# Optimization experiments

Measured on AMD Instinct MI355X. Metric: run time of the kernel, lower is better.

The kernel has to match this reference:

```python
import jax, jax.numpy as jnp
import numpy as np

P, M, N, D, H, DFF = 20000, 20000, 16, 128, 8, 512
DPH = D // H
EPS = 1e-6
LN_EPS = 1e-5


def vn_linear(x, w):
    # x: (..., C_in, 3), w: (C_in, C_out) -> (..., C_out, 3)
    return jnp.einsum('...ci,co->...oi', x, w)


def vn_layernorm(x, gamma, beta):
    # x: (P, D, 3); layernorm over channel dim on vector norms, rescale directions
    n = jnp.linalg.norm(x, axis=-1)                      # (P, D)
    mu = jnp.mean(n, axis=-1, keepdims=True)
    var = jnp.var(n, axis=-1, keepdims=True)
    n_hat = (n - mu) / jnp.sqrt(var + LN_EPS) * gamma + beta
    return x * (n_hat / (n + EPS))[..., None]


def vn_relu(q, k):
    # VN nonlinearity: q, k: (..., C, 3); project q off negative half-space of k
    dot = jnp.sum(q * k, axis=-1, keepdims=True)         # (..., C, 1)
    ksq = jnp.sum(k * k, axis=-1, keepdims=True)
    return jnp.where(dot >= 0, q, q - (dot / (ksq + EPS)) * k)


def setup_inputs():
    key = jax.random.key(0)
    ks = jax.random.split(key, 24)
    s = lambda i, shp, scale: (jax.random.normal(ks[i], shp, jnp.float32) * scale)
    inp = {
        'tgt': s(0, (P, D * 3), 1.0),
        'memory': s(1, (M, D * 3), 1.0),
        'sh': s(2, (P, N + 1, 3), 1.0),
        'dist_atten': s(3, (P, N, H), 1.0),
        'Wq': s(4, (D, D), D ** -0.5),
        'Wk': s(5, (D, D), D ** -0.5),
        'Wv': s(6, (D, D), D ** -0.5),
        'Wo': s(7, (D, D), D ** -0.5),
        'g_w1': s(8, (D, H), D ** -0.5),
        'g_b1': jnp.zeros((H,), jnp.float32),
        'g_w2': s(9, (H, H), H ** -0.5),
        'g_b2': jnp.zeros((H,), jnp.float32),
        'ln1_g': jnp.ones((D,), jnp.float32),
        'ln1_b': jnp.zeros((D,), jnp.float32),
        'ln2_g': jnp.ones((D,), jnp.float32),
        'ln2_b': jnp.zeros((D,), jnp.float32),
        'ff_w1': s(10, (D, DFF), D ** -0.5),
        'ff_d1': s(11, (D, DFF), D ** -0.5),
        'ff_w2': s(12, (DFF, D), DFF ** -0.5),
        'index_pair': jax.random.randint(ks[13], (P, N), 0, M),
        'cnt1': jax.random.randint(ks[14], (P,), 0, N),
        'cnt2': jax.random.randint(ks[15], (P,), 0, N),
    }
    return inp


def reference(tgt, memory, sh, dist_atten, Wq, Wk, Wv, Wo,
              g_w1, g_b1, g_w2, g_b2, ln1_g, ln1_b, ln2_g, ln2_b,
              ff_w1, ff_d1, ff_w2, index_pair, cnt1, cnt2):
    x = tgt.reshape(P, D, 3)
    mem = memory.reshape(M, D, 3)
    q = vn_linear(x, Wq)                                  # (P, D, 3)
    k_all = vn_linear(mem, Wk)                            # (M, D, 3)
    v_all = vn_linear(mem, Wv)
    # irregular neighbor gather (ca_attention_mapper_v3)
    k = k_all[index_pair]                                 # (P, N, D, 3)
    v = v_all[index_pair]                                 # (P, N, D, 3)
    sh_n = sh[:, 1:].reshape(P, N, 1, 3)                  # drop l=0 term
    # multi-head dot attention on 3D vector features
    dot_atten = jnp.einsum('phdi,pnhdi->pnh',
                           q.reshape(P, H, DPH, 3),
                           k.reshape(P, N, H, DPH, 3))
    # spherical-harmonic position bias
    pos = jnp.sum((k - q[:, None]) * sh_n, axis=-1)       # (P, N, D)
    pos = jax.nn.relu(pos @ g_w1 + g_b1) @ g_w2 + g_b2    # (P, N, H)
    atten = (dot_atten + pos + dist_atten) / (DPH ** 0.5)
    atten = jax.nn.softmax(atten, axis=1)                 # softmax over neighbors
    tgt2 = jnp.einsum('pnh,pnhci->phci', atten,
                      v.reshape(P, N, H, DPH, 3)).reshape(P, D, 3)
    tgt2 = vn_linear(tgt2, Wo)
    y = vn_layernorm(x + tgt2, ln1_g, ln1_b)
    h1 = vn_relu(vn_linear(y, ff_w1), vn_linear(y, ff_d1))
    ff_out = vn_linear(h1, ff_w2)
    y = vn_layernorm(y + ff_out, ln2_g, ln2_b)
    return y.reshape(P, D * 3)
```

## Files before the change

### kernel.cpp

```cpp
#include <hip/hip_runtime.h>

#define PP 20000

typedef short short8 __attribute__((ext_vector_type(8)));
typedef float floatx4 __attribute__((ext_vector_type(4)));

__device__ __forceinline__ unsigned int bf16_rne_bits(float x){
    unsigned int xb = __float_as_uint(x);
    return (xb + 0x7FFFu + ((xb >> 16) & 1u)) & 0xFFFF0000u;
}
__device__ __forceinline__ void split2(float x, short &h, short &l){
    unsigned int hb = bf16_rne_bits(x);
    h = (short)(hb >> 16);
    float r = x - __uint_as_float(hb);
    l = (short)(bf16_rne_bits(r) >> 16);
}

__device__ __align__(16) short g_ff1[32*8192];
__device__ __align__(16) short g_ff2[16*8192];
__device__ __align__(16) short g_qkvo[4][4*8192];

__global__ __launch_bounds__(256) void prep_weights(
    const float* __restrict__ Wq, const float* __restrict__ Wk,
    const float* __restrict__ Wv, const float* __restrict__ Wo,
    const float* __restrict__ W1, const float* __restrict__ Wd,
    const float* __restrict__ W2)
{
    const int tid = blockIdx.x*256 + threadIdx.x;
    for (int e = tid; e < 65536; e += 16384){
        int j = e & 7, kg = (e>>3) & 15, n = (e>>7) & 15, ch = e >> 11;
        int k = kg*8 + j, col = ch*16 + n;
        int pos = n*128 + ((kg ^ (n&7)) << 3) + j;
        short h, l;
        split2(W1[(size_t)k*512 + col], h, l);
        g_ff1[ch*8192 + pos]        = h;
        g_ff1[ch*8192 + 2048 + pos] = l;
        split2(Wd[(size_t)k*512 + col], h, l);
        g_ff1[ch*8192 + 4096 + pos] = h;
        g_ff1[ch*8192 + 6144 + pos] = l;
    }
    for (int e = tid; e < 65536; e += 16384){
        int w = e & 31, n2 = (e>>5) & 127, pair = e >> 12;
        int lslot = (w>>3) ^ ((n2>>1)&3);
        int k = pair*32 + lslot*8 + (w&7);
        short h, l; split2(W2[(size_t)k*128 + n2], h, l);
        g_ff2[pair*8192 + n2*32 + w]        = h;
        g_ff2[pair*8192 + 4096 + n2*32 + w] = l;
    }
    for (int e = tid; e < 65536; e += 16384){
        int w = e & 127, col = (e>>7) & 31, ch = (e>>12) & 3, wg = e >> 14;
        int lslot = (w>>3) ^ (col&7);
        int k = lslot*8 + (w&7);
        const float* Wsrc = (wg==0)?Wq:(wg==1)?Wk:(wg==2)?Wv:Wo;
        short h, l; split2(Wsrc[(size_t)k*128 + ch*32 + col], h, l);
        g_qkvo[wg][ch*8192 + col*128 + w]        = h;
        g_qkvo[wg][ch*8192 + 4096 + col*128 + w] = l;
    }
}

__global__ __launch_bounds__(256) void vn_gemm_mfma(const float* __restrict__ in,
    int widx, float* __restrict__ out)
{
    __shared__ __align__(16) char pool[32768];
    short* Ysh = (short*)pool;
    short* Ysl = (short*)(pool + 16384);
    short* Bh  = (short*)pool;
    short* Bl  = (short*)(pool + 8192);

    const int tid  = threadIdx.x;
    const int wv   = tid >> 6;
    const int lane = tid & 63;
    const int mrow = lane & 15;
    const int kgrp = lane >> 4;
    const int p0   = blockIdx.x * 16;

    for (int f = tid; f < 2048; f += 256){
        int row = (f >> 7)*4 + 3, k = f & 127;
        Ysh[row*128 + k] = 0; Ysl[row*128 + k] = 0;
    }
    #pragma unroll
    for (int t = 0; t < 6; ++t){
        int f = tid + t*256;
        float4 w4 = *(const float4*)(in + (size_t)p0*384 + f*4);
        int e = f*4, pl = e/384, rem = e - pl*384;
        float vv4[4] = {w4.x, w4.y, w4.z, w4.w};
        #pragma unroll
        for (int j=0;j<4;++j){
            int c = (rem+j)/3, i = (rem+j) - c*3;
            int row = pl*4 + i;
            int idx = row*128 + (((c>>3) ^ (row&7)) << 3) + (c&7);
            short h, l; split2(vv4[j], h, l);
            Ysh[idx] = h; Ysl[idx] = l;
        }
    }
    __syncthreads();
    short8 ahf[4], alf[4];
    {
        const int arow = wv*16 + mrow;
        #pragma unroll
        for (int ks=0;ks<4;++ks){
            int slot = ks*4 + kgrp;
            int aoff = arow*128 + ((slot ^ (arow&7)) << 3);
            ahf[ks] = *(const short8*)(Ysh + aoff);
            alf[ks] = *(const short8*)(Ysl + aoff);
        }
    }

    const short* gW = g_qkvo[widx];
    for (int ch = 0; ch < 4; ++ch){
        __syncthreads();
        #pragma unroll
        for (int t=0;t<4;++t)
            ((short8*)pool)[tid + t*256] =
                ((const short8*)(gW + ch*8192))[tid + t*256];
        __syncthreads();

        #pragma unroll
        for (int ntl=0; ntl<2; ++ntl){
            floatx4 acc = {0.f,0.f,0.f,0.f};
            const int lcol = ntl*16 + mrow;
            #pragma unroll
            for (int ks=0;ks<4;++ks){
                int slot = ks*4 + kgrp;
                int boff = lcol*128 + ((slot ^ (mrow&7)) << 3);
                short8 bh = *(const short8*)(Bh + boff);
                short8 bl = *(const short8*)(Bl + boff);
                acc = __builtin_amdgcn_mfma_f32_16x16x32_bf16(ahf[ks], bh, acc, 0,0,0);
                acc = __builtin_amdgcn_mfma_f32_16x16x32_bf16(ahf[ks], bl, acc, 0,0,0);
                acc = __builtin_amdgcn_mfma_f32_16x16x32_bf16(alf[ks], bh, acc, 0,0,0);
            }
            const int p = p0 + wv*4 + kgrp;
            const int o = ch*32 + ntl*16 + mrow;
            size_t base = (size_t)p*384 + (size_t)o*3;
            out[base    ] = acc[0];
            out[base + 1] = acc[1];
            out[base + 2] = acc[2];
        }
    }
}

__global__ __launch_bounds__(128) void attn_score(
    const float* qf, const float* __restrict__ kf,
    const float* __restrict__ sh, const float* __restrict__ dist, const int* __restrict__ idxp,
    const float* __restrict__ gw1, const float* __restrict__ gb1,
    const float* __restrict__ gw2, const float* __restrict__ gb2,
    float* att)
{
    const int p = blockIdx.x, c = threadIdx.x;
    __shared__ __align__(16) float dot_s[16*132];
    __shared__ __align__(16) float pos_s[16*132];
    __shared__ float sh_s[48];
    __shared__ int   nidx[16];
    __shared__ __align__(16) float w1t[8*132];
    __shared__ float w2_s[64], b1_s[8], b2_s[8];
    __shared__ float u2_s[16*8], logit_s[16*8];

    if (c < 16) nidx[c] = idxp[p*16 + c];
    if (c < 48) sh_s[c] = sh[(size_t)p*51 + 3 + c];
    #pragma unroll
    for (int f = c; f < 1024; f += 128){
        int th2 = f >> 7, cc2 = f & 127;
        w1t[th2*132 + cc2] = gw1[cc2*8 + th2];
    }
    if (c < 64) w2_s[c] = gw2[c];
    if (c < 8){ b1_s[c]=gb1[c]; b2_s[c]=gb2[c]; }
    size_t qa = (size_t)p*384 + c*3;
    float qx = qf[qa], qy = qf[qa+1], qz = qf[qa+2];
    __syncthreads();

    for (int n=0;n<16;++n){
        size_t kbase = (size_t)nidx[n]*384 + c*3;
        float kx = kf[kbase], ky = kf[kbase+1], kz = kf[kbase+2];
        dot_s[n*132 + c] = kx*qx + ky*qy + kz*qz;
        pos_s[n*132 + c] = (kx-qx)*sh_s[n*3] + (ky-qy)*sh_s[n*3+1] + (kz-qz)*sh_s[n*3+2];
    }
    __syncthreads();

    const int tn = c >> 3, th = c & 7;
    const float* drow = dot_s + tn*132 + th*16;
    float4 d0 = *(const float4*)(drow);
    float4 d1 = *(const float4*)(drow + 4);
    float4 d2 = *(const float4*)(drow + 8);
    float4 d3 = *(const float4*)(drow + 12);
    float dsum = (d0.x+d0.y+d0.z+d0.w) + (d1.x+d1.y+d1.z+d1.w)
               + (d2.x+d2.y+d2.z+d2.w) + (d3.x+d3.y+d3.z+d3.w);

    float uj = b1_s[th];
    const float* prow = pos_s + tn*132;
    const float* wrow = w1t  + th*132;
    #pragma unroll 8
    for (int cc=0; cc<128; cc+=4){
        float4 pv = *(const float4*)(prow + cc);
        float4 wv = *(const float4*)(wrow + cc);
        uj = fmaf(pv.x, wv.x, uj);
        uj = fmaf(pv.y, wv.y, uj);
        uj = fmaf(pv.z, wv.z, uj);
        uj = fmaf(pv.w, wv.w, uj);
    }
    u2_s[tn*8+th] = fmaxf(uj, 0.f);
    __syncthreads();

    float l = b2_s[th];
    #pragma unroll
    for (int j=0;j<8;++j) l += u2_s[tn*8+j]*w2_s[j*8+th];
    l += dsum + dist[(size_t)p*128 + tn*8 + th];
    logit_s[tn*8+th] = l * 0.25f;
    __syncthreads();

    if (c < 8){
        float mx = -3.0e38f;
        #pragma unroll
        for (int n=0;n<16;++n) mx = fmaxf(mx, logit_s[n*8+c]);
        float e[16], ssum = 0.f;
        #pragma unroll
        for (int n=0;n<16;++n){ e[n] = __expf(logit_s[n*8+c]-mx); ssum += e[n]; }
        float inv = 1.f/ssum;
        #pragma unroll
        for (int n=0;n<16;++n) att[(size_t)p*384 + n*8 + c] = e[n]*inv;
    }
}

__global__ __launch_bounds__(128) void attn_apply(const float* __restrict__ vv,
                                                  const int* __restrict__ idxp,
                                                  float* io)
{
    const int p = blockIdx.x, c = threadIdx.x;
    __shared__ float att_s[128];
    __shared__ int   nidx[16];
    if (c < 16) nidx[c] = idxp[p*16 + c];
    att_s[c] = io[(size_t)p*384 + c];
    __syncthreads();

    const int h = c >> 4;
    float ax=0.f, ay=0.f, az=0.f;
    #pragma unroll
    for (int n=0;n<16;++n){
        float wgt = att_s[n*8+h];
        size_t vb = (size_t)nidx[n]*384 + c*3;
        ax += wgt*vv[vb]; ay += wgt*vv[vb+1]; az += wgt*vv[vb+2];
    }
    size_t ob = (size_t)p*384 + c*3;
    io[ob] = ax; io[ob+1] = ay; io[ob+2] = az;
}

__global__ __launch_bounds__(256,2) void vn_ff_mfma(const float* __restrict__ in,
    const float* __restrict__ l2g, const float* __restrict__ l2b,
    float* __restrict__ out)
{
    __shared__ __align__(16) char pool[40960];
    short* Ws1h = (short*)(pool);
    short* Ws1l = (short*)(pool + 4096);
    short* Wsdh = (short*)(pool + 8192);
    short* Wsdl = (short*)(pool + 12288);
    short* Ws2h = (short*)(pool + 16384);
    short* Ws2l = (short*)(pool + 24576);
    short* Hsh  = (short*)(pool + 32768);
    short* Hsl  = (short*)(pool + 36864);
    short* Ysh  = (short*)(pool);
    short* Ysl  = (short*)(pool + 16384);

    const int tid  = threadIdx.x;
    const int wv   = tid >> 6;
    const int lane = tid & 63;
    const int mrow = lane & 15;
    const int kgrp = lane >> 4;
    const int p0   = blockIdx.x * 16;

    for (int f = tid; f < 2048; f += 256){
        int row = (f >> 7)*4 + 3, k = f & 127;
        Ysh[row*128 + k] = 0; Ysl[row*128 + k] = 0;
    }
    #pragma unroll
    for (int t = 0; t < 6; ++t){
        int f = tid + t*256;
        float4 w4 = *(const float4*)(in + (size_t)p0*384 + f*4);
        int e = f*4, pl = e/384, rem = e - pl*384;
        float vv4[4] = {w4.x, w4.y, w4.z, w4.w};
        #pragma unroll
        for (int j=0;j<4;++j){
            int c = (rem+j)/3, i = (rem+j) - c*3;
            int row = pl*4 + i;
            int idx = row*128 + (((c>>3) ^ (row&7)) << 3) + (c&7);
            short h, l; split2(vv4[j], h, l);
            Ysh[idx] = h; Ysl[idx] = l;
        }
    }
    __syncthreads();
    short8 ahf[4], alf[4];
    {
        const int arow = wv*16 + mrow;
        #pragma unroll
        for (int ks=0;ks<4;++ks){
            int slot = ks*4 + kgrp;
            int aoff = arow*128 + ((slot ^ (arow&7)) << 3);
            ahf[ks] = *(const short8*)(Ysh + aoff);
            alf[ks] = *(const short8*)(Ysl + aoff);
        }
    }

    floatx4 acc2[8];
    #pragma unroll
    for (int nt=0;nt<8;++nt) acc2[nt] = (floatx4){0.f,0.f,0.f,0.f};

    for (int ch = 0; ch < 32; ++ch){
        __syncthreads();
        #pragma unroll
        for (int t=0;t<4;++t)
            ((short8*)pool)[tid + t*256] =
                ((const short8*)(g_ff1 + ch*8192))[tid + t*256];
        if ((ch & 1) == 0){
            #pragma unroll
            for (int t=0;t<4;++t)
                ((short8*)(pool + 16384))[tid + t*256] =
                    ((const short8*)(g_ff2 + (ch>>1)*8192))[tid + t*256];
        }
        __syncthreads();

        floatx4 aU = {0.f,0.f,0.f,0.f}, aD = {0.f,0.f,0.f,0.f};
        #pragma unroll
        for (int ks=0;ks<4;++ks){
            int slot = ks*4 + kgrp;
            int boff = mrow*128 + ((slot ^ (mrow&7)) << 3);
            short8 b1h = *(const short8*)(Ws1h + boff);
            short8 b1l = *(const short8*)(Ws1l + boff);
            short8 bdh = *(const short8*)(Wsdh + boff);
            short8 bdl = *(const short8*)(Wsdl + boff);
            aU = __builtin_amdgcn_mfma_f32_16x16x32_bf16(ahf[ks], b1h, aU, 0,0,0);
            aU = __builtin_amdgcn_mfma_f32_16x16x32_bf16(ahf[ks], b1l, aU, 0,0,0);
            aU = __builtin_amdgcn_mfma_f32_16x16x32_bf16(alf[ks], b1h, aU, 0,0,0);
            aD = __builtin_amdgcn_mfma_f32_16x16x32_bf16(ahf[ks], bdh, aD, 0,0,0);
            aD = __builtin_amdgcn_mfma_f32_16x16x32_bf16(ahf[ks], bdl, aD, 0,0,0);
            aD = __builtin_amdgcn_mfma_f32_16x16x32_bf16(alf[ks], bdh, aD, 0,0,0);
        }

        {
            float ux=aU[0], uy=aU[1], uz=aU[2];
            float dx=aD[0], dy=aD[1], dz=aD[2];
            float dot = ux*dx + uy*dy + uz*dz;
            float ksq = dx*dx + dy*dy + dz*dz;
            if (dot < 0.f){
                float fc = dot/(ksq + 1e-6f);
                ux -= fc*dx; uy -= fc*dy; uz -= fc*dz;
            }
            int col  = (ch & 1)*16 + mrow;
            int slot = col >> 3, cl = col & 7;
            float hv[4] = {ux, uy, uz, 0.f};
            #pragma unroll
            for (int r=0;r<4;++r){
                int row = wv*16 + kgrp*4 + r;
                int idx = row*32 + ((slot ^ ((row>>1)&3)) << 3) + cl;
                short h, l; split2(hv[r], h, l);
                Hsh[idx] = h; Hsl[idx] = l;
            }
        }

        if (ch & 1){
            const int arow2 = wv*16 + mrow;
            int aoff = arow2*32 + ((kgrp ^ ((arow2>>1)&3)) << 3);
            short8 ah = *(const short8*)(Hsh + aoff);
            short8 al = *(const short8*)(Hsl + aoff);
            #pragma unroll
            for (int nt=0;nt<8;++nt){
                int bcol = nt*16 + mrow;
                int boff = bcol*32 + ((kgrp ^ ((bcol>>1)&3)) << 3);
                short8 bh = *(const short8*)(Ws2h + boff);
                short8 bl = *(const short8*)(Ws2l + boff);
                acc2[nt] = __builtin_amdgcn_mfma_f32_16x16x32_bf16(ah, bh, acc2[nt], 0,0,0);
                acc2[nt] = __builtin_amdgcn_mfma_f32_16x16x32_bf16(ah, bl, acc2[nt], 0,0,0);
                acc2[nt] = __builtin_amdgcn_mfma_f32_16x16x32_bf16(al, bh, acc2[nt], 0,0,0);
            }
        }
    }

    const int p = p0 + wv*4 + kgrp;
    float nrm[8];
    float s1 = 0.f, s2 = 0.f;
    #pragma unroll
    for (int nt=0;nt<8;++nt){
        int o = nt*16 + mrow;
        size_t base = (size_t)p*384 + (size_t)o*3;
        float rx = in[base]   + acc2[nt][0];
        float ry = in[base+1] + acc2[nt][1];
        float rz = in[base+2] + acc2[nt][2];
        float n = sqrtf(rx*rx + ry*ry + rz*rz);
        nrm[nt] = n;
        s1 += n; s2 += n*n;
    }
    #pragma unroll
    for (int m=1; m<16; m<<=1){
        s1 += __shfl_xor(s1, m);
        s2 += __shfl_xor(s2, m);
    }
    float mu  = s1*(1.f/128.f);
    float var = s2*(1.f/128.f) - mu*mu;
    float inv = rsqrtf(var + 1e-5f);
    #pragma unroll
    for (int nt=0;nt<8;++nt){
        int o = nt*16 + mrow;
        size_t base = (size_t)p*384 + (size_t)o*3;
        float rx = in[base]   + acc2[nt][0];
        float ry = in[base+1] + acc2[nt][1];
        float rz = in[base+2] + acc2[nt][2];
        float nh = (nrm[nt] - mu)*inv*l2g[o] + l2b[o];
        float sc = nh/(nrm[nt] + 1e-6f);
        out[base] = rx*sc; out[base+1] = ry*sc; out[base+2] = rz*sc;
    }
}

__global__ __launch_bounds__(256) void vn_ln(const float* __restrict__ a, const float* b2,
                                             const float* __restrict__ gamma, const float* __restrict__ beta,
                                             float* out)
{
    const int tid = threadIdx.x;
    const int pl = tid >> 7, c = tid & 127;
    const int p = blockIdx.x*2 + pl;
    size_t base = (size_t)p*384 + c*3;
    float rx = a[base]   + b2[base];
    float ry = a[base+1] + b2[base+1];
    float rz = a[base+2] + b2[base+2];
    float nc = sqrtf(rx*rx + ry*ry + rz*rz);
    float s1 = nc, s2 = nc*nc;
    for (int off=32; off; off>>=1){ s1 += __shfl_down(s1, off); s2 += __shfl_down(s2, off); }
    __shared__ float pr[4][2];
    if ((tid & 63) == 0){ pr[tid>>6][0] = s1; pr[tid>>6][1] = s2; }
    __syncthreads();
    float S1 = pr[pl*2][0] + pr[pl*2+1][0];
    float S2 = pr[pl*2][1] + pr[pl*2+1][1];
    float mu  = S1*(1.f/128.f);
    float var = S2*(1.f/128.f) - mu*mu;
    float nh = (nc - mu)*rsqrtf(var + 1e-5f)*gamma[c] + beta[c];
    float sc = nh/(nc + 1e-6f);
    out[base] = rx*sc; out[base+1] = ry*sc; out[base+2] = rz*sc;
}

extern "C" void kernel_launch(void* const* d_in, const int* in_sizes, int n_in,
                              void* d_out, int out_size, void* d_ws, size_t ws_size,
                              hipStream_t stream)
{
    const float* tgt  = (const float*)d_in[0];
    const float* mem  = (const float*)d_in[1];
    const float* sh   = (const float*)d_in[2];
    const float* dist = (const float*)d_in[3];
    const float* Wq   = (const float*)d_in[4];
    const float* Wk   = (const float*)d_in[5];
    const float* Wv   = (const float*)d_in[6];
    const float* Wo   = (const float*)d_in[7];
    const float* gw1  = (const float*)d_in[8];
    const float* gb1  = (const float*)d_in[9];
    const float* gw2  = (const float*)d_in[10];
    const float* gb2  = (const float*)d_in[11];
    const float* ln1g = (const float*)d_in[12];
    const float* ln1b = (const float*)d_in[13];
    const float* ln2g = (const float*)d_in[14];
    const float* ln2b = (const float*)d_in[15];
    const float* fw1  = (const float*)d_in[16];
    const float* fd1  = (const float*)d_in[17];
    const float* fw2  = (const float*)d_in[18];
    const int*   idx  = (const int*)d_in[19];

    float* wsf = (float*)d_ws;
    float* outf = (float*)d_out;

    prep_weights<<<64,256,0,stream>>>(Wq, Wk, Wv, Wo, fw1, fd1, fw2);

    vn_gemm_mfma<<<1250,256,0,stream>>>(mem, 1, wsf);
    vn_gemm_mfma<<<1250,256,0,stream>>>(tgt, 0, outf);
    attn_score<<<PP,128,0,stream>>>(outf, wsf, sh, dist, idx, gw1, gb1, gw2, gb2, outf);
    vn_gemm_mfma<<<1250,256,0,stream>>>(mem, 2, wsf);
    attn_apply<<<PP,128,0,stream>>>(wsf, idx, outf);
    vn_gemm_mfma<<<1250,256,0,stream>>>(outf, 3, wsf);
    vn_ln<<<PP/2,256,0,stream>>>(tgt, wsf, ln1g, ln1b, wsf);
    vn_ff_mfma<<<1250,256,0,stream>>>(wsf, ln2g, ln2b, outf);
}
```

Measured before the change: 504.5 us.

## Process two 16-point tiles per block in VN feed-forward kernel

The FF kernel now handles 32 points per block instead of 16, so each block runs two M-tiles against every staged weight chunk. The goal is to halve the global-to-LDS traffic for the FF1/FF2 weights and the barriers per point. The cost is more accumulator registers (two sets of acc2), more LDS (48KB), and half as many blocks (625), which can lower occupancy and leave CUs underfilled.

```diff
diff --git a/kernel.cpp b/kernel.cpp
--- a/kernel.cpp
+++ b/kernel.cpp
@@ -247,7 +247,7 @@
     const float* __restrict__ l2g, const float* __restrict__ l2b,
     float* __restrict__ out)
 {
-    __shared__ __align__(16) char pool[40960];
+    __shared__ __align__(16) char pool[49152];
     short* Ws1h = (short*)(pool);
     short* Ws1l = (short*)(pool + 4096);
     short* Wsdh = (short*)(pool + 8192);
@@ -255,7 +255,7 @@
     short* Ws2h = (short*)(pool + 16384);
     short* Ws2l = (short*)(pool + 24576);
     short* Hsh  = (short*)(pool + 32768);
-    short* Hsl  = (short*)(pool + 36864);
+    short* Hsl  = (short*)(pool + 40960);
     short* Ysh  = (short*)(pool);
     short* Ysl  = (short*)(pool + 16384);
 
@@ -264,43 +264,47 @@
     const int lane = tid & 63;
     const int mrow = lane & 15;
     const int kgrp = lane >> 4;
-    const int p0   = blockIdx.x * 16;
-
-    for (int f = tid; f < 2048; f += 256){
-        int row = (f >> 7)*4 + 3, k = f & 127;
-        Ysh[row*128 + k] = 0; Ysl[row*128 + k] = 0;
-    }
-    #pragma unroll
-    for (int t = 0; t < 6; ++t){
-        int f = tid + t*256;
-        float4 w4 = *(const float4*)(in + (size_t)p0*384 + f*4);
-        int e = f*4, pl = e/384, rem = e - pl*384;
-        float vv4[4] = {w4.x, w4.y, w4.z, w4.w};
-        #pragma unroll
-        for (int j=0;j<4;++j){
-            int c = (rem+j)/3, i = (rem+j) - c*3;
-            int row = pl*4 + i;
-            int idx = row*128 + (((c>>3) ^ (row&7)) << 3) + (c&7);
-            short h, l; split2(vv4[j], h, l);
-            Ysh[idx] = h; Ysl[idx] = l;
-        }
-    }
-    __syncthreads();
-    short8 ahf[4], alf[4];
-    {
+    const int p0   = blockIdx.x * 32;
+
+    short8 ahf[2][4], alf[2][4];
+    #pragma unroll
+    for (int hp = 0; hp < 2; ++hp){
+        __syncthreads();
+        for (int f = tid; f < 2048; f += 256){
+            int row = (f >> 7)*4 + 3, k = f & 127;
+            Ysh[row*128 + k] = 0; Ysl[row*128 + k] = 0;
+        }
+        #pragma unroll
+        for (int t = 0; t < 6; ++t){
+            int f = tid + t*256;
+            float4 w4 = *(const float4*)(in + ((size_t)p0 + hp*16)*384 + f*4);
+            int e = f*4, pl = e/384, rem = e - pl*384;
+            float vv4[4] = {w4.x, w4.y, w4.z, w4.w};
+            #pragma unroll
+            for (int j=0;j<4;++j){
+                int c = (rem+j)/3, i = (rem+j) - c*3;
+                int row = pl*4 + i;
+                int idx = row*128 + (((c>>3) ^ (row&7)) << 3) + (c&7);
+                short h, l; split2(vv4[j], h, l);
+                Ysh[idx] = h; Ysl[idx] = l;
+            }
+        }
+        __syncthreads();
         const int arow = wv*16 + mrow;
         #pragma unroll
         for (int ks=0;ks<4;++ks){
             int slot = ks*4 + kgrp;
             int aoff = arow*128 + ((slot ^ (arow&7)) << 3);
-            ahf[ks] = *(const short8*)(Ysh + aoff);
-            alf[ks] = *(const short8*)(Ysl + aoff);
-        }
-    }
-
-    floatx4 acc2[8];
-    #pragma unroll
-    for (int nt=0;nt<8;++nt) acc2[nt] = (floatx4){0.f,0.f,0.f,0.f};
+            ahf[hp][ks] = *(const short8*)(Ysh + aoff);
+            alf[hp][ks] = *(const short8*)(Ysl + aoff);
+        }
+    }
+
+    floatx4 acc2[2][8];
+    #pragma unroll
+    for (int mt=0;mt<2;++mt)
+        #pragma unroll
+        for (int nt=0;nt<8;++nt) acc2[mt][nt] = (floatx4){0.f,0.f,0.f,0.f};
 
     for (int ch = 0; ch < 32; ++ch){
         __syncthreads();
@@ -316,7 +320,10 @@
         }
         __syncthreads();
 
-        floatx4 aU = {0.f,0.f,0.f,0.f}, aD = {0.f,0.f,0.f,0.f};
+        floatx4 aU[2], aD[2];
+        #pragma unroll
+        for (int mt=0;mt<2;++mt){ aU[mt] = (floatx4){0.f,0.f,0.f,0.f};
+                                  aD[mt] = (floatx4){0.f,0.f,0.f,0.f}; }
         #pragma unroll
         for (int ks=0;ks<4;++ks){
             int slot = ks*4 + kgrp;
@@ -325,17 +332,21 @@
             short8 b1l = *(const short8*)(Ws1l + boff);
             short8 bdh = *(const short8*)(Wsdh + boff);
             short8 bdl = *(const short8*)(Wsdl + boff);
-            aU = __builtin_amdgcn_mfma_f32_16x16x32_bf16(ahf[ks], b1h, aU, 0,0,0);
-            aU = __builtin_amdgcn_mfma_f32_16x16x32_bf16(ahf[ks], b1l, aU, 0,0,0);
-            aU = __builtin_amdgcn_mfma_f32_16x16x32_bf16(alf[ks], b1h, aU, 0,0,0);
-            aD = __builtin_amdgcn_mfma_f32_16x16x32_bf16(ahf[ks], bdh, aD, 0,0,0);
-            aD = __builtin_amdgcn_mfma_f32_16x16x32_bf16(ahf[ks], bdl, aD, 0,0,0);
-            aD = __builtin_amdgcn_mfma_f32_16x16x32_bf16(alf[ks], bdh, aD, 0,0,0);
-        }
-
-        {
-            float ux=aU[0], uy=aU[1], uz=aU[2];
-            float dx=aD[0], dy=aD[1], dz=aD[2];
+            #pragma unroll
+            for (int mt=0;mt<2;++mt){
+                aU[mt] = __builtin_amdgcn_mfma_f32_16x16x32_bf16(ahf[mt][ks], b1h, aU[mt], 0,0,0);
+                aU[mt] = __builtin_amdgcn_mfma_f32_16x16x32_bf16(ahf[mt][ks], b1l, aU[mt], 0,0,0);
+                aU[mt] = __builtin_amdgcn_mfma_f32_16x16x32_bf16(alf[mt][ks], b1h, aU[mt], 0,0,0);
+                aD[mt] = __builtin_amdgcn_mfma_f32_16x16x32_bf16(ahf[mt][ks], bdh, aD[mt], 0,0,0);
+                aD[mt] = __builtin_amdgcn_mfma_f32_16x16x32_bf16(ahf[mt][ks], bdl, aD[mt], 0,0,0);
+                aD[mt] = __builtin_amdgcn_mfma_f32_16x16x32_bf16(alf[mt][ks], bdh, aD[mt], 0,0,0);
+            }
+        }
+
+        #pragma unroll
+        for (int mt=0;mt<2;++mt){
+            float ux=aU[mt][0], uy=aU[mt][1], uz=aU[mt][2];
+            float dx=aD[mt][0], dy=aD[mt][1], dz=aD[mt][2];
             float dot = ux*dx + uy*dy + uz*dz;
             float ksq = dx*dx + dy*dy + dz*dz;
             if (dot < 0.f){
@@ -347,7 +358,7 @@
             float hv[4] = {ux, uy, uz, 0.f};
             #pragma unroll
             for (int r=0;r<4;++r){
-                int row = wv*16 + kgrp*4 + r;
+                int row = mt*64 + wv*16 + kgrp*4 + r;
                 int idx = row*32 + ((slot ^ ((row>>1)&3)) << 3) + cl;
                 short h, l; split2(hv[r], h, l);
                 Hsh[idx] = h; Hsl[idx] = l;
@@ -355,55 +366,65 @@
         }
 
         if (ch & 1){
-            const int arow2 = wv*16 + mrow;
-            int aoff = arow2*32 + ((kgrp ^ ((arow2>>1)&3)) << 3);
-            short8 ah = *(const short8*)(Hsh + aoff);
-            short8 al = *(const short8*)(Hsl + aoff);
+            short8 ah[2], al[2];
+            #pragma unroll
+            for (int mt=0;mt<2;++mt){
+                int arow2 = mt*64 + wv*16 + mrow;
+                int aoff = arow2*32 + ((kgrp ^ ((arow2>>1)&3)) << 3);
+                ah[mt] = *(const short8*)(Hsh + aoff);
+                al[mt] = *(const short8*)(Hsl + aoff);
+            }
             #pragma unroll
             for (int nt=0;nt<8;++nt){
                 int bcol = nt*16 + mrow;
                 int boff = bcol*32 + ((kgrp ^ ((bcol>>1)&3)) << 3);
                 short8 bh = *(const short8*)(Ws2h + boff);
                 short8 bl = *(const short8*)(Ws2l + boff);
-                acc2[nt] = __builtin_amdgcn_mfma_f32_16x16x32_bf16(ah, bh, acc2[nt], 0,0,0);
-                acc2[nt] = __builtin_amdgcn_mfma_f32_16x16x32_bf16(ah, bl, acc2[nt], 0,0,0);
-                acc2[nt] = __builtin_amdgcn_mfma_f32_16x16x32_bf16(al, bh, acc2[nt], 0,0,0);
-            }
-        }
-    }
-
-    const int p = p0 + wv*4 + kgrp;
-    float nrm[8];
-    float s1 = 0.f, s2 = 0.f;
-    #pragma unroll
-    for (int nt=0;nt<8;++nt){
-        int o = nt*16 + mrow;
-        size_t base = (size_t)p*384 + (size_t)o*3;
-        float rx = in[base]   + acc2[nt][0];
-        float ry = in[base+1] + acc2[nt][1];
-        float rz = in[base+2] + acc2[nt][2];
-        float n = sqrtf(rx*rx + ry*ry + rz*rz);
-        nrm[nt] = n;
-        s1 += n; s2 += n*n;
-    }
-    #pragma unroll
-    for (int m=1; m<16; m<<=1){
-        s1 += __shfl_xor(s1, m);
-        s2 += __shfl_xor(s2, m);
-    }
-    float mu  = s1*(1.f/128.f);
-    float var = s2*(1.f/128.f) - mu*mu;
-    float inv = rsqrtf(var + 1e-5f);
-    #pragma unroll
-    for (int nt=0;nt<8;++nt){
-        int o = nt*16 + mrow;
-        size_t base = (size_t)p*384 + (size_t)o*3;
-        float rx = in[base]   + acc2[nt][0];
-        float ry = in[base+1] + acc2[nt][1];
-        float rz = in[base+2] + acc2[nt][2];
-        float nh = (nrm[nt] - mu)*inv*l2g[o] + l2b[o];
-        float sc = nh/(nrm[nt] + 1e-6f);
-        out[base] = rx*sc; out[base+1] = ry*sc; out[base+2] = rz*sc;
+                #pragma unroll
+                for (int mt=0;mt<2;++mt){
+                    acc2[mt][nt] = __builtin_amdgcn_mfma_f32_16x16x32_bf16(ah[mt], bh, acc2[mt][nt], 0,0,0);
+                    acc2[mt][nt] = __builtin_amdgcn_mfma_f32_16x16x32_bf16(ah[mt], bl, acc2[mt][nt], 0,0,0);
+                    acc2[mt][nt] = __builtin_amdgcn_mfma_f32_16x16x32_bf16(al[mt], bh, acc2[mt][nt], 0,0,0);
+                }
+            }
+        }
+    }
+
+    #pragma unroll
+    for (int mt=0;mt<2;++mt){
+        const int p = p0 + mt*16 + wv*4 + kgrp;
+        float nrm[8];
+        float s1 = 0.f, s2 = 0.f;
+        #pragma unroll
+        for (int nt=0;nt<8;++nt){
+            int o = nt*16 + mrow;
+            size_t base = (size_t)p*384 + (size_t)o*3;
+            float rx = in[base]   + acc2[mt][nt][0];
+            float ry = in[base+1] + acc2[mt][nt][1];
+            float rz = in[base+2] + acc2[mt][nt][2];
+            float n = sqrtf(rx*rx + ry*ry + rz*rz);
+            nrm[nt] = n;
+            s1 += n; s2 += n*n;
+        }
+        #pragma unroll
+        for (int m=1; m<16; m<<=1){
+            s1 += __shfl_xor(s1, m);
+            s2 += __shfl_xor(s2, m);
+        }
+        float mu  = s1*(1.f/128.f);
+        float var = s2*(1.f/128.f) - mu*mu;
+        float inv = rsqrtf(var + 1e-5f);
+        #pragma unroll
+        for (int nt=0;nt<8;++nt){
+            int o = nt*16 + mrow;
+            size_t base = (size_t)p*384 + (size_t)o*3;
+            float rx = in[base]   + acc2[mt][nt][0];
+            float ry = in[base+1] + acc2[mt][nt][1];
+            float rz = in[base+2] + acc2[mt][nt][2];
+            float nh = (nrm[nt] - mu)*inv*l2g[o] + l2b[o];
+            float sc = nh/(nrm[nt] + 1e-6f);
+            out[base] = rx*sc; out[base+1] = ry*sc; out[base+2] = rz*sc;
+        }
     }
 }
 
@@ -470,5 +491,5 @@
     attn_apply<<<PP,128,0,stream>>>(wsf, idx, outf);
     vn_gemm_mfma<<<1250,256,0,stream>>>(outf, 3, wsf);
     vn_ln<<<PP/2,256,0,stream>>>(tgt, wsf, ln1g, ln1b, wsf);
-    vn_ff_mfma<<<1250,256,0,stream>>>(wsf, ln2g, ln2b, outf);
-}
+    vn_ff_mfma<<<625,256,0,stream>>>(wsf, ln2g, ln2b, outf);
+}
```

New measurement: 581.9 us. +15.4%, slower.
